# Kernel tuning notes

Hardware: AMD Instinct MI355X
Metric: run time of the kernel (lower is better)

## Reference

```python
import jax, jax.numpy as jnp
import numpy as np

DIM = 1024
HEADS = 16
HEAD_DIM = DIM // HEADS
B, S = 4, 2048


def setup_inputs() -> dict:
    key = jax.random.key(0)
    ks = jax.random.split(key, 12)
    scale = 1.0 / np.sqrt(DIM)
    inp = {
        "q": jax.random.normal(ks[0], (B, S, DIM), jnp.float32),
        "k": jax.random.normal(ks[1], (B, S, DIM), jnp.float32),
        "v": jax.random.normal(ks[2], (B, S, DIM), jnp.float32),
        "Wq": jax.random.normal(ks[3], (DIM, DIM), jnp.float32) * scale,
        "bq": jax.random.normal(ks[4], (DIM,), jnp.float32) * 0.01,
        "Wk": jax.random.normal(ks[5], (DIM, DIM), jnp.float32) * scale,
        "bk": jax.random.normal(ks[6], (DIM,), jnp.float32) * 0.01,
        "Wv": jax.random.normal(ks[7], (DIM, DIM), jnp.float32) * scale,
        "bv": jax.random.normal(ks[8], (DIM,), jnp.float32) * 0.01,
        "Wo": jax.random.normal(ks[9], (DIM, DIM), jnp.float32) * scale,
        "bo": jax.random.normal(ks[10], (DIM,), jnp.float32) * 0.01,
        "mask": jax.random.randint(ks[11], (B, S, S), 0, 2, jnp.int32),
    }
    return inp


def reference(q, k, v, Wq, bq, Wk, bk, Wv, bv, Wo, bo, mask):
    # QKV projections, split into heads: [B, H, S, Dh]
    def proj(x, W, b):
        y = x @ W + b
        return y.reshape(B, S, HEADS, HEAD_DIM).transpose(0, 2, 1, 3)

    qh, kh, vh = proj(q, Wq, bq), proj(k, Wk, bk), proj(v, Wv, bv)

    # scaled dot-product attention with additive mask fill (-1e9 where mask==0)
    score = jnp.einsum('bhqd,bhkd->bhqk', qh, kh) / jnp.sqrt(jnp.float32(HEAD_DIM))
    score = jnp.where(mask[:, None, :, :] == 0, jnp.float32(-1e9), score)
    attn = jax.nn.softmax(score, axis=-1)  # dropout p=0.0 -> identity

    out = jnp.einsum('bhqk,bhkd->bhqd', attn, vh)
    out = out.transpose(0, 2, 1, 3).reshape(B, S, DIM)
    return out @ Wo + bo
```

## Files before the change

### kernel.cpp

```cpp
#include <hip/hip_runtime.h>
#include <cstdint>
#include <cstddef>

#define BB 4
#define SS 2048
#define DIMM 1024
#define NH 16
#define DH 64
#define MT 8192

typedef __attribute__((ext_vector_type(8))) short bf16x8;
typedef __attribute__((ext_vector_type(4))) float f32x4;
typedef __attribute__((ext_vector_type(4))) unsigned short u16x4;
typedef __attribute__((ext_vector_type(4))) unsigned int uint32x4;

#define MFMA_BF16(a, b, c) __builtin_amdgcn_mfma_f32_16x16x32_bf16(a, b, c, 0, 0, 0)

#define QSCALE 0.1803368801111137f

__device__ __forceinline__ unsigned int cvtpk(float lo, float hi) {
    unsigned int r;
    asm("v_cvt_pk_bf16_f32 %0, %1, %2" : "=v"(r) : "v"(lo), "v"(hi));
    return r;
}

__device__ __forceinline__ unsigned short f2b1(float f) {
    return (unsigned short)cvtpk(f, f);
}

__device__ __forceinline__ float fexp2(float x) {
    float r;
    asm("v_exp_f32 %0, %1" : "=v"(r) : "v"(x));
    return r;
}

__device__ __forceinline__ void gload16(const void* g, void* l) {
    __builtin_amdgcn_global_load_lds(
        (const __attribute__((address_space(1))) unsigned int*)g,
        (__attribute__((address_space(3))) unsigned int*)l, 16, 0, 0);
}

__device__ __forceinline__ int swzb(int row, int cb) {
    return row * 128 + (((cb) ^ (row & 7)) << 4);
}

__global__ __launch_bounds__(256)
void prep_kernel(const float* __restrict__ q, const float* __restrict__ k,
                 const float* __restrict__ v,
                 unsigned short* __restrict__ Qb, unsigned short* __restrict__ Kb,
                 unsigned short* __restrict__ Vb,
                 const int* __restrict__ mask, unsigned long long* __restrict__ mp,
                 const float* __restrict__ Wq, const float* __restrict__ Wk,
                 const float* __restrict__ Wv, const float* __restrict__ Wo,
                 unsigned short* __restrict__ WT3, unsigned short* __restrict__ WTo)
{
    __shared__ unsigned short T[64][72];
    const int tid = threadIdx.x;
    const int bid = blockIdx.x;

    if (bid < 12288) {
        const int which = bid >> 12;
        const float* src = (which == 0) ? q : (which == 1) ? k : v;
        unsigned short* dst = (which == 0) ? Qb : (which == 1) ? Kb : Vb;
        const size_t i = ((size_t)(bid & 4095) * 256 + tid) * 8;
        const float4 lo = *reinterpret_cast<const float4*>(src + i);
        const float4 hi = *reinterpret_cast<const float4*>(src + i + 4);
        uint32x4 w = {cvtpk(lo.x, lo.y), cvtpk(lo.z, lo.w),
                      cvtpk(hi.x, hi.y), cvtpk(hi.z, hi.w)};
        *reinterpret_cast<uint32x4*>(dst + i) = w;
    } else if (bid < 77824) {
        const size_t i = (size_t)(bid - 12288) * 256 + tid;
        const unsigned long long bal = __ballot(mask[i] != 0);
        if ((tid & 63) == 0) mp[i >> 6] = bal;
    } else {
        const int wb = bid - 77824;
        const int which = wb >> 8;
        const float* W = (which == 0) ? Wq : (which == 1) ? Wk : (which == 2) ? Wv : Wo;
        unsigned short* WT = (which < 3) ? (WT3 + (size_t)which * DIMM * DIMM) : WTo;
        const float scale = (which == 0) ? QSCALE : 1.0f;
        const int within = wb & 255;
        const int n0 = (within & 15) * 64, k0 = (within >> 4) * 64;
#pragma unroll
        for (int it = 0; it < 4; ++it) {
            const int c = tid + it * 256;
            const int row = c >> 4, c4 = (c & 15) * 4;
            const float4 vv = *reinterpret_cast<const float4*>(
                &W[(size_t)(k0 + row) * DIMM + n0 + c4]);
            T[row][c4 + 0] = f2b1(vv.x * scale);
            T[row][c4 + 1] = f2b1(vv.y * scale);
            T[row][c4 + 2] = f2b1(vv.z * scale);
            T[row][c4 + 3] = f2b1(vv.w * scale);
        }
        __syncthreads();
#pragma unroll
        for (int it = 0; it < 4; ++it) {
            const int c = tid + it * 256;
            const int n = c >> 4, k4 = (c & 15) * 4;
            u16x4 o;
            o[0] = T[k4 + 0][n];
            o[1] = T[k4 + 1][n];
            o[2] = T[k4 + 2][n];
            o[3] = T[k4 + 3][n];
            *reinterpret_cast<u16x4*>(&WT[(size_t)(n0 + n) * DIMM + k0 + k4]) = o;
        }
    }
}

__global__ __launch_bounds__(256)
void gemm_qkv_kernel(const unsigned short* __restrict__ Qb,
                     const unsigned short* __restrict__ Kb,
                     const unsigned short* __restrict__ Vb,
                     const unsigned short* __restrict__ WT3,
                     const float* __restrict__ bq, const float* __restrict__ bk,
                     const float* __restrict__ bv,
                     unsigned short* __restrict__ Qh, unsigned short* __restrict__ Kh,
                     unsigned short* __restrict__ VhT)
{
    __shared__ __align__(16) unsigned short As[128 * 32];
    __shared__ __align__(16) unsigned short Bs[128 * 32];
    const int tid = threadIdx.x;
    const int w = tid >> 6, l = tid & 63;
    const int g = l >> 4, li = l & 15;
    const int bid = blockIdx.x;
    const int region = bid >> 9;
    const int rl = bid & 511;
    const int swz = (rl & 7) * 64 + (rl >> 3);
    const int m0 = (swz >> 3) * 128, n0 = (swz & 7) * 128;
    const int wm0 = (w >> 1) * 64, wn0 = (w & 1) * 64;

    const unsigned short* A = (region == 0) ? Qb : (region == 1) ? Kb : Vb;
    const unsigned short* BT = WT3 + (size_t)region * (DIMM * DIMM);

    const f32x4 fzero = {0.f, 0.f, 0.f, 0.f};
    f32x4 acc[4][4];
#pragma unroll
    for (int i = 0; i < 4; ++i)
#pragma unroll
        for (int j = 0; j < 4; ++j) acc[i][j] = fzero;

    for (int k0 = 0; k0 < DIMM; k0 += 32) {
#pragma unroll
        for (int it = 0; it < 2; ++it) {
            const int c = it * 256 + w * 64 + l;
            const int row = c >> 2, cb = c & 3;
            gload16(&A[(size_t)(m0 + row) * DIMM + k0 + cb * 8],
                    &As[(it * 256 + w * 64) * 8]);
        }
#pragma unroll
        for (int it = 0; it < 2; ++it) {
            const int c = it * 256 + w * 64 + l;
            const int row = c >> 2, cb = c & 3;
            gload16(&BT[(size_t)(n0 + row) * DIMM + k0 + cb * 8],
                    &Bs[(it * 256 + w * 64) * 8]);
        }
        __syncthreads();

        bf16x8 af[4], bf[4];
#pragma unroll
        for (int mb = 0; mb < 4; ++mb)
            af[mb] = *reinterpret_cast<const bf16x8*>(&As[(wm0 + mb * 16 + li) * 32 + g * 8]);
#pragma unroll
        for (int nb = 0; nb < 4; ++nb)
            bf[nb] = *reinterpret_cast<const bf16x8*>(&Bs[(wn0 + nb * 16 + li) * 32 + g * 8]);
#pragma unroll
        for (int mb = 0; mb < 4; ++mb)
#pragma unroll
            for (int nb = 0; nb < 4; ++nb)
                acc[mb][nb] = MFMA_BF16(af[mb], bf[nb], acc[mb][nb]);
        __syncthreads();
    }

    const float* bias = (region == 0) ? bq : (region == 1) ? bk : bv;
    const float bscale = (region == 0) ? QSCALE : 1.0f;
    float bv4[4];
#pragma unroll
    for (int nb = 0; nb < 4; ++nb)
        bv4[nb] = bias[n0 + wn0 + nb * 16 + li] * bscale;

    unsigned short* dst = (region == 0) ? Qh : (region == 1) ? Kh : VhT;
#pragma unroll
    for (int mb = 0; mb < 4; ++mb) {
#pragma unroll
        for (int r = 0; r < 4; ++r) {
            const int row_g = m0 + wm0 + mb * 16 + g * 4 + r;
#pragma unroll
            for (int nb = 0; nb < 4; ++nb) {
                const int col = n0 + wn0 + nb * 16 + li;
                const float val = acc[mb][nb][r] + bv4[nb];
                const int bb = row_g >> 11, s = row_g & 2047;
                const int hh = col >> 6, dd = col & 63;
                if (region < 2) {
                    dst[(((size_t)(bb * NH + hh)) * SS + s) * DH + dd] = f2b1(val);
                } else {
                    const int st = s & 63;
                    const int sp = (st & 32) + ((st >> 2) & 3) * 8 + ((st & 16) >> 2) + (st & 3);
                    dst[(((size_t)(bb * NH + hh)) * DH + dd) * SS + (s & ~63) + sp] = f2b1(val);
                }
            }
        }
    }
}

__global__ __launch_bounds__(256)
void gemm_out_kernel(const unsigned short* __restrict__ Ax, const unsigned short* __restrict__ BT,
                     const float* __restrict__ bias, float* __restrict__ Y)
{
    __shared__ __align__(16) unsigned short As[128 * 32];
    __shared__ __align__(16) unsigned short Bs[128 * 32];
    const int tid = threadIdx.x;
    const int w = tid >> 6, l = tid & 63;
    const int g = l >> 4, li = l & 15;
    const int bid = blockIdx.x;
    const int swz = (bid & 7) * 64 + (bid >> 3);
    const int m0 = (swz >> 3) * 128, n0 = (swz & 7) * 128;
    const int wm0 = (w >> 1) * 64, wn0 = (w & 1) * 64;

    const f32x4 fzero = {0.f, 0.f, 0.f, 0.f};
    f32x4 acc[4][4];
#pragma unroll
    for (int i = 0; i < 4; ++i)
#pragma unroll
        for (int j = 0; j < 4; ++j) acc[i][j] = fzero;

    for (int k0 = 0; k0 < DIMM; k0 += 32) {
        const int h = k0 >> 6;
#pragma unroll
        for (int it = 0; it < 2; ++it) {
            const int c = it * 256 + w * 64 + l;
            const int row = c >> 2, cb = c & 3;
            const int m = m0 + row;
            const int bb = m >> 11, s = m & 2047;
            gload16(&Ax[(((size_t)(bb * NH + h)) * SS + s) * DH + (k0 & 63) + cb * 8],
                    &As[(it * 256 + w * 64) * 8]);
        }
#pragma unroll
        for (int it = 0; it < 2; ++it) {
            const int c = it * 256 + w * 64 + l;
            const int row = c >> 2, cb = c & 3;
            gload16(&BT[(size_t)(n0 + row) * DIMM + k0 + cb * 8],
                    &Bs[(it * 256 + w * 64) * 8]);
        }
        __syncthreads();

        bf16x8 af[4], bf[4];
#pragma unroll
        for (int mb = 0; mb < 4; ++mb)
            af[mb] = *reinterpret_cast<const bf16x8*>(&As[(wm0 + mb * 16 + li) * 32 + g * 8]);
#pragma unroll
        for (int nb = 0; nb < 4; ++nb)
            bf[nb] = *reinterpret_cast<const bf16x8*>(&Bs[(wn0 + nb * 16 + li) * 32 + g * 8]);
#pragma unroll
        for (int mb = 0; mb < 4; ++mb)
#pragma unroll
            for (int nb = 0; nb < 4; ++nb)
                acc[mb][nb] = MFMA_BF16(af[mb], bf[nb], acc[mb][nb]);
        __syncthreads();
    }

    float bv4[4];
#pragma unroll
    for (int nb = 0; nb < 4; ++nb)
        bv4[nb] = bias[n0 + wn0 + nb * 16 + li];

#pragma unroll
    for (int mb = 0; mb < 4; ++mb) {
#pragma unroll
        for (int r = 0; r < 4; ++r) {
            const int row_g = m0 + wm0 + mb * 16 + g * 4 + r;
#pragma unroll
            for (int nb = 0; nb < 4; ++nb) {
                const int col = n0 + wn0 + nb * 16 + li;
                Y[(size_t)row_g * DIMM + col] = acc[mb][nb][r] + bv4[nb];
            }
        }
    }
}

__global__ __launch_bounds__(256, 4)
void flash_kernel(const unsigned short* __restrict__ Qh, const unsigned short* __restrict__ Kh,
                  const unsigned short* __restrict__ VhT, const unsigned long long* __restrict__ maskp,
                  unsigned short* __restrict__ Ctx)
{
    const int h = blockIdx.x, qt = blockIdx.y, b = blockIdx.z;
    const int tid = threadIdx.x;
    const int w = tid >> 6, l = tid & 63;
    const int g = l >> 4, li = l & 15;

    __shared__ __align__(16) unsigned short smem[4 * 64 * 64];
    __shared__ unsigned int LUT4[4];

    const int q0 = qt * 128;
    const size_t hb = ((size_t)(b * NH + h)) * (size_t)(SS * DH);

    if (tid < 4) LUT4[tid] = ((tid & 1) ? 0xFFFFu : 0u) | ((tid & 2) ? 0xFFFF0000u : 0u);

    bf16x8 qf[2][2];
#pragma unroll
    for (int qc = 0; qc < 2; ++qc) {
        const unsigned short* qp = &Qh[hb + (size_t)(q0 + w * 32 + qc * 16 + li) * DH + g * 8];
        qf[qc][0] = *reinterpret_cast<const bf16x8*>(qp);
        qf[qc][1] = *reinterpret_cast<const bf16x8*>(qp + 32);
    }

    bf16x8 vones;
#pragma unroll
    for (int j = 0; j < 8; ++j) vones[j] = (short)0x3F80;

    const f32x4 fzero = {0.f, 0.f, 0.f, 0.f};
    f32x4 oacc[2][4];
    f32x4 lacc[2];
#pragma unroll
    for (int qc = 0; qc < 2; ++qc) {
        lacc[qc] = fzero;
#pragma unroll
        for (int mb = 0; mb < 4; ++mb) oacc[qc][mb] = fzero;
    }

    int ks_[2], vs_[2];
#pragma unroll
    for (int it = 0; it < 2; ++it) {
        const int c = it * 256 + w * 64 + l;
        const int row = c >> 3, cb = (c & 7) ^ (row & 7);
        ks_[it] = row * DH + cb * 8;
        vs_[it] = row * SS + cb * 8;
    }
    const unsigned short* Ksrc = Kh + hb;
    const unsigned short* Vsrc = VhT + hb;
    const unsigned long long* mrow_p = maskp + ((size_t)(b * SS + q0 + w * 32 + li)) * 32;

#define STAGE(bn, tt) do {                                                      \
    gload16(Ksrc + (size_t)(tt) * 4096 + ks_[0], smem + (bn) * 4096 + w * 512); \
    gload16(Ksrc + (size_t)(tt) * 4096 + ks_[1], smem + (bn) * 4096 + 2048 + w * 512); \
    gload16(Vsrc + (size_t)(tt) * 64 + vs_[0], smem + 8192 + (bn) * 4096 + w * 512);   \
    gload16(Vsrc + (size_t)(tt) * 64 + vs_[1], smem + 8192 + (bn) * 4096 + 2048 + w * 512); \
} while (0)

    STAGE(0, 0);
    __syncthreads();

    int buf = 0;
    for (int t = 0; t < SS / 64; ++t) {
        if (t < SS / 64 - 1) STAGE(buf ^ 1, t + 1);

        const unsigned long long mw0 = mrow_p[t];
        const unsigned long long mw1 = mrow_p[512 + t];

        const char* Kc = (const char*)(smem + buf * 4096);
        bf16x8 kf[4][2];
#pragma unroll
        for (int nb = 0; nb < 4; ++nb)
#pragma unroll
            for (int hh = 0; hh < 2; ++hh)
                kf[nb][hh] = *reinterpret_cast<const bf16x8*>(
                    Kc + (nb * 16 + li) * 128 + (((hh * 4 + g) ^ (li & 7)) << 4));

        bf16x8 pf[2][2];
#pragma unroll
        for (int qc = 0; qc < 2; ++qc) {
            f32x4 st[4];
#pragma unroll
            for (int nb = 0; nb < 4; ++nb) st[nb] = fzero;
            __builtin_amdgcn_s_setprio(1);
#pragma unroll
            for (int nb = 0; nb < 4; ++nb)
#pragma unroll
                for (int hh = 0; hh < 2; ++hh)
                    st[nb] = MFMA_BF16(kf[nb][hh], qf[qc][hh], st[nb]);
            __builtin_amdgcn_s_setprio(0);

            float e[4][4];
#pragma unroll
            for (int nb = 0; nb < 4; ++nb)
#pragma unroll
                for (int r = 0; r < 4; ++r)
                    e[nb][r] = fexp2(st[nb][r]);

            const unsigned long long msh = (qc ? mw1 : mw0) >> (g * 4);
            const unsigned lo = (unsigned)msh, hi = (unsigned)(msh >> 32);
            uint32x4 w0 = {cvtpk(e[0][0], e[0][1]), cvtpk(e[0][2], e[0][3]),
                           cvtpk(e[1][0], e[1][1]), cvtpk(e[1][2], e[1][3])};
            uint32x4 w1 = {cvtpk(e[2][0], e[2][1]), cvtpk(e[2][2], e[2][3]),
                           cvtpk(e[3][0], e[3][1]), cvtpk(e[3][2], e[3][3])};
            w0[0] &= LUT4[lo & 3u];         w0[1] &= LUT4[(lo >> 2) & 3u];
            w0[2] &= LUT4[(lo >> 16) & 3u]; w0[3] &= LUT4[(lo >> 18) & 3u];
            w1[0] &= LUT4[hi & 3u];         w1[1] &= LUT4[(hi >> 2) & 3u];
            w1[2] &= LUT4[(hi >> 16) & 3u]; w1[3] &= LUT4[(hi >> 18) & 3u];
            pf[qc][0] = __builtin_bit_cast(bf16x8, w0);
            pf[qc][1] = __builtin_bit_cast(bf16x8, w1);
        }

        const char* Vc = (const char*)(smem + 8192 + buf * 4096);
        bf16x8 vf[4][2];
#pragma unroll
        for (int mb = 0; mb < 4; ++mb)
#pragma unroll
            for (int hh = 0; hh < 2; ++hh)
                vf[mb][hh] = *reinterpret_cast<const bf16x8*>(
                    Vc + (mb * 16 + li) * 128 + (((hh * 4 + g) ^ (li & 7)) << 4));

#pragma unroll
        for (int qc = 0; qc < 2; ++qc) {
            __builtin_amdgcn_s_setprio(1);
#pragma unroll
            for (int hh = 0; hh < 2; ++hh)
#pragma unroll
                for (int mb = 0; mb < 4; ++mb)
                    oacc[qc][mb] = MFMA_BF16(pf[qc][hh], vf[mb][hh], oacc[qc][mb]);
            lacc[qc] = MFMA_BF16(pf[qc][0], vones, lacc[qc]);
            lacc[qc] = MFMA_BF16(pf[qc][1], vones, lacc[qc]);
            __builtin_amdgcn_s_setprio(0);
        }

        __syncthreads();
        buf ^= 1;
    }
#undef STAGE

    unsigned short* Ps = smem;
#pragma unroll
    for (int qc = 0; qc < 2; ++qc) {
#pragma unroll
        for (int r = 0; r < 4; ++r) {
            const int row = w * 32 + qc * 16 + g * 4 + r;
            const float linv = 1.0f / lacc[qc][r];
#pragma unroll
            for (int mb = 0; mb < 4; ++mb) {
                const int dd = mb * 16 + li;
                *(unsigned short*)((char*)Ps + swzb(row, dd >> 3) + (dd & 7) * 2) =
                    f2b1(oacc[qc][mb][r] * linv);
            }
        }
    }
    __syncthreads();
#pragma unroll
    for (int it = 0; it < 4; ++it) {
        const int c = it * 64 + l;
        const int qrow = w * 32 + (c >> 3), cb = c & 7;
        const bf16x8 ov = *reinterpret_cast<const bf16x8*>((const char*)Ps + swzb(qrow, cb));
        *reinterpret_cast<bf16x8*>(&Ctx[hb + (size_t)(q0 + qrow) * DH + cb * 8]) = ov;
    }
}

extern "C" void kernel_launch(void* const* d_in, const int* in_sizes, int n_in,
                              void* d_out, int out_size, void* d_ws, size_t ws_size,
                              hipStream_t stream)
{
    const float* q  = (const float*)d_in[0];
    const float* k  = (const float*)d_in[1];
    const float* v  = (const float*)d_in[2];
    const float* Wq = (const float*)d_in[3];
    const float* bq = (const float*)d_in[4];
    const float* Wk = (const float*)d_in[5];
    const float* bk = (const float*)d_in[6];
    const float* Wv = (const float*)d_in[7];
    const float* bv = (const float*)d_in[8];
    const float* Wo = (const float*)d_in[9];
    const float* bo = (const float*)d_in[10];
    const int* mask = (const int*)d_in[11];
    float* out = (float*)d_out;

    const size_t M1 = 1048576, M8 = (size_t)MT * DIMM;
    unsigned short* WT3 = (unsigned short*)d_ws;
    unsigned short* WTo = WT3 + 3 * M1;
    unsigned short* Qb  = WTo + M1;
    unsigned short* Kb  = Qb + M8;
    unsigned short* Vb  = Kb + M8;
    unsigned short* Qh  = Vb + M8;
    unsigned short* Kh  = Qh + M8;
    unsigned long long* maskp = (unsigned long long*)(Kh + M8);
    unsigned short* VhT = (unsigned short*)(maskp + (size_t)BB * SS * SS / 64);
    unsigned short* Ctx = Kb;

    dim3 blk(256);

    prep_kernel<<<dim3(78848), blk, 0, stream>>>(q, k, v, Qb, Kb, Vb,
                                                 mask, maskp,
                                                 Wq, Wk, Wv, Wo, WT3, WTo);

    gemm_qkv_kernel<<<dim3(1536), blk, 0, stream>>>(Qb, Kb, Vb, WT3, bq, bk, bv,
                                                    Qh, Kh, VhT);

    dim3 fgrid(NH, SS / 128, BB);
    flash_kernel<<<fgrid, blk, 0, stream>>>(Qh, Kh, VhT, maskp, Ctx);

    gemm_out_kernel<<<dim3(512), blk, 0, stream>>>(Ctx, WTo, bo, out);
}
```

Measured before the change: 274.7 us.

## Drop LDS K/V staging in flash kernel, load fragments directly from global

New measurement: 639.2 us. 2.33x slower.

```diff
diff --git a/kernel.cpp b/kernel.cpp
--- a/kernel.cpp
+++ b/kernel.cpp
@@ -276,7 +276,7 @@
     }
 }
 
-__global__ __launch_bounds__(256, 4)
+__global__ __launch_bounds__(256, 5)
 void flash_kernel(const unsigned short* __restrict__ Qh, const unsigned short* __restrict__ Kh,
                   const unsigned short* __restrict__ VhT, const unsigned long long* __restrict__ maskp,
                   unsigned short* __restrict__ Ctx)
@@ -286,20 +286,20 @@
     const int w = tid >> 6, l = tid & 63;
     const int g = l >> 4, li = l & 15;
 
-    __shared__ __align__(16) unsigned short smem[4 * 64 * 64];
+    __shared__ __align__(16) unsigned short Ps[64 * 64];
     __shared__ unsigned int LUT4[4];
 
-    const int q0 = qt * 128;
+    const int q0 = qt * 64;
     const size_t hb = ((size_t)(b * NH + h)) * (size_t)(SS * DH);
 
     if (tid < 4) LUT4[tid] = ((tid & 1) ? 0xFFFFu : 0u) | ((tid & 2) ? 0xFFFF0000u : 0u);
-
-    bf16x8 qf[2][2];
-#pragma unroll
-    for (int qc = 0; qc < 2; ++qc) {
-        const unsigned short* qp = &Qh[hb + (size_t)(q0 + w * 32 + qc * 16 + li) * DH + g * 8];
-        qf[qc][0] = *reinterpret_cast<const bf16x8*>(qp);
-        qf[qc][1] = *reinterpret_cast<const bf16x8*>(qp + 32);
+    __syncthreads();
+
+    bf16x8 qf[2];
+    {
+        const unsigned short* qp = &Qh[hb + (size_t)(q0 + w * 16 + li) * DH + g * 8];
+        qf[0] = *reinterpret_cast<const bf16x8*>(qp);
+        qf[1] = *reinterpret_cast<const bf16x8*>(qp + 32);
     }
 
     bf16x8 vones;
@@ -307,135 +307,93 @@
     for (int j = 0; j < 8; ++j) vones[j] = (short)0x3F80;
 
     const f32x4 fzero = {0.f, 0.f, 0.f, 0.f};
-    f32x4 oacc[2][4];
-    f32x4 lacc[2];
-#pragma unroll
-    for (int qc = 0; qc < 2; ++qc) {
-        lacc[qc] = fzero;
-#pragma unroll
-        for (int mb = 0; mb < 4; ++mb) oacc[qc][mb] = fzero;
-    }
-
-    int ks_[2], vs_[2];
-#pragma unroll
-    for (int it = 0; it < 2; ++it) {
-        const int c = it * 256 + w * 64 + l;
-        const int row = c >> 3, cb = (c & 7) ^ (row & 7);
-        ks_[it] = row * DH + cb * 8;
-        vs_[it] = row * SS + cb * 8;
-    }
-    const unsigned short* Ksrc = Kh + hb;
-    const unsigned short* Vsrc = VhT + hb;
-    const unsigned long long* mrow_p = maskp + ((size_t)(b * SS + q0 + w * 32 + li)) * 32;
-
-#define STAGE(bn, tt) do {                                                      \
-    gload16(Ksrc + (size_t)(tt) * 4096 + ks_[0], smem + (bn) * 4096 + w * 512); \
-    gload16(Ksrc + (size_t)(tt) * 4096 + ks_[1], smem + (bn) * 4096 + 2048 + w * 512); \
-    gload16(Vsrc + (size_t)(tt) * 64 + vs_[0], smem + 8192 + (bn) * 4096 + w * 512);   \
-    gload16(Vsrc + (size_t)(tt) * 64 + vs_[1], smem + 8192 + (bn) * 4096 + 2048 + w * 512); \
-} while (0)
-
-    STAGE(0, 0);
-    __syncthreads();
-
-    int buf = 0;
+    f32x4 oacc[4];
+    f32x4 lacc = fzero;
+#pragma unroll
+    for (int mb = 0; mb < 4; ++mb) oacc[mb] = fzero;
+
+    const unsigned short* Kl = Kh + hb + (size_t)li * DH + g * 8;
+    const unsigned short* Vl = VhT + hb + (size_t)li * SS + g * 8;
+    const unsigned long long* mrow_p = maskp + ((size_t)(b * SS + q0 + w * 16 + li)) * 32;
+
     for (int t = 0; t < SS / 64; ++t) {
-        if (t < SS / 64 - 1) STAGE(buf ^ 1, t + 1);
-
-        const unsigned long long mw0 = mrow_p[t];
-        const unsigned long long mw1 = mrow_p[512 + t];
-
-        const char* Kc = (const char*)(smem + buf * 4096);
+        const unsigned long long mw = mrow_p[t];
+
+        const unsigned short* Kt = Kl + t * 4096;
         bf16x8 kf[4][2];
 #pragma unroll
         for (int nb = 0; nb < 4; ++nb)
 #pragma unroll
             for (int hh = 0; hh < 2; ++hh)
-                kf[nb][hh] = *reinterpret_cast<const bf16x8*>(
-                    Kc + (nb * 16 + li) * 128 + (((hh * 4 + g) ^ (li & 7)) << 4));
-
-        bf16x8 pf[2][2];
-#pragma unroll
-        for (int qc = 0; qc < 2; ++qc) {
-            f32x4 st[4];
-#pragma unroll
-            for (int nb = 0; nb < 4; ++nb) st[nb] = fzero;
-            __builtin_amdgcn_s_setprio(1);
-#pragma unroll
-            for (int nb = 0; nb < 4; ++nb)
-#pragma unroll
-                for (int hh = 0; hh < 2; ++hh)
-                    st[nb] = MFMA_BF16(kf[nb][hh], qf[qc][hh], st[nb]);
-            __builtin_amdgcn_s_setprio(0);
-
-            float e[4][4];
-#pragma unroll
-            for (int nb = 0; nb < 4; ++nb)
-#pragma unroll
-                for (int r = 0; r < 4; ++r)
-                    e[nb][r] = fexp2(st[nb][r]);
-
-            const unsigned long long msh = (qc ? mw1 : mw0) >> (g * 4);
-            const unsigned lo = (unsigned)msh, hi = (unsigned)(msh >> 32);
-            uint32x4 w0 = {cvtpk(e[0][0], e[0][1]), cvtpk(e[0][2], e[0][3]),
-                           cvtpk(e[1][0], e[1][1]), cvtpk(e[1][2], e[1][3])};
-            uint32x4 w1 = {cvtpk(e[2][0], e[2][1]), cvtpk(e[2][2], e[2][3]),
-                           cvtpk(e[3][0], e[3][1]), cvtpk(e[3][2], e[3][3])};
-            w0[0] &= LUT4[lo & 3u];         w0[1] &= LUT4[(lo >> 2) & 3u];
-            w0[2] &= LUT4[(lo >> 16) & 3u]; w0[3] &= LUT4[(lo >> 18) & 3u];
-            w1[0] &= LUT4[hi & 3u];         w1[1] &= LUT4[(hi >> 2) & 3u];
-            w1[2] &= LUT4[(hi >> 16) & 3u]; w1[3] &= LUT4[(hi >> 18) & 3u];
-            pf[qc][0] = __builtin_bit_cast(bf16x8, w0);
-            pf[qc][1] = __builtin_bit_cast(bf16x8, w1);
-        }
-
-        const char* Vc = (const char*)(smem + 8192 + buf * 4096);
+                kf[nb][hh] = *reinterpret_cast<const bf16x8*>(Kt + nb * 1024 + hh * 32);
+
+        f32x4 st[4];
+#pragma unroll
+        for (int nb = 0; nb < 4; ++nb) st[nb] = fzero;
+        __builtin_amdgcn_s_setprio(1);
+#pragma unroll
+        for (int nb = 0; nb < 4; ++nb)
+#pragma unroll
+            for (int hh = 0; hh < 2; ++hh)
+                st[nb] = MFMA_BF16(kf[nb][hh], qf[hh], st[nb]);
+        __builtin_amdgcn_s_setprio(0);
+
+        float e[4][4];
+#pragma unroll
+        for (int nb = 0; nb < 4; ++nb)
+#pragma unroll
+            for (int r = 0; r < 4; ++r)
+                e[nb][r] = fexp2(st[nb][r]);
+
+        const unsigned long long msh = mw >> (g * 4);
+        const unsigned lo = (unsigned)msh, hi = (unsigned)(msh >> 32);
+        uint32x4 w0 = {cvtpk(e[0][0], e[0][1]), cvtpk(e[0][2], e[0][3]),
+                       cvtpk(e[1][0], e[1][1]), cvtpk(e[1][2], e[1][3])};
+        uint32x4 w1 = {cvtpk(e[2][0], e[2][1]), cvtpk(e[2][2], e[2][3]),
+                       cvtpk(e[3][0], e[3][1]), cvtpk(e[3][2], e[3][3])};
+        w0[0] &= LUT4[lo & 3u];         w0[1] &= LUT4[(lo >> 2) & 3u];
+        w0[2] &= LUT4[(lo >> 16) & 3u]; w0[3] &= LUT4[(lo >> 18) & 3u];
+        w1[0] &= LUT4[hi & 3u];         w1[1] &= LUT4[(hi >> 2) & 3u];
+        w1[2] &= LUT4[(hi >> 16) & 3u]; w1[3] &= LUT4[(hi >> 18) & 3u];
+        bf16x8 pf[2];
+        pf[0] = __builtin_bit_cast(bf16x8, w0);
+        pf[1] = __builtin_bit_cast(bf16x8, w1);
+
+        const unsigned short* Vt = Vl + t * 64;
         bf16x8 vf[4][2];
 #pragma unroll
         for (int mb = 0; mb < 4; ++mb)
 #pragma unroll
             for (int hh = 0; hh < 2; ++hh)
                 vf[mb][hh] = *reinterpret_cast<const bf16x8*>(
-                    Vc + (mb * 16 + li) * 128 + (((hh * 4 + g) ^ (li & 7)) << 4));
-
-#pragma unroll
-        for (int qc = 0; qc < 2; ++qc) {
-            __builtin_amdgcn_s_setprio(1);
-#pragma unroll
-            for (int hh = 0; hh < 2; ++hh)
-#pragma unroll
-                for (int mb = 0; mb < 4; ++mb)
-                    oacc[qc][mb] = MFMA_BF16(pf[qc][hh], vf[mb][hh], oacc[qc][mb]);
-            lacc[qc] = MFMA_BF16(pf[qc][0], vones, lacc[qc]);
-            lacc[qc] = MFMA_BF16(pf[qc][1], vones, lacc[qc]);
-            __builtin_amdgcn_s_setprio(0);
-        }
-
-        __syncthreads();
-        buf ^= 1;
-    }
-#undef STAGE
-
-    unsigned short* Ps = smem;
-#pragma unroll
-    for (int qc = 0; qc < 2; ++qc) {
-#pragma unroll
-        for (int r = 0; r < 4; ++r) {
-            const int row = w * 32 + qc * 16 + g * 4 + r;
-            const float linv = 1.0f / lacc[qc][r];
-#pragma unroll
-            for (int mb = 0; mb < 4; ++mb) {
-                const int dd = mb * 16 + li;
-                *(unsigned short*)((char*)Ps + swzb(row, dd >> 3) + (dd & 7) * 2) =
-                    f2b1(oacc[qc][mb][r] * linv);
-            }
-        }
-    }
-    __syncthreads();
-#pragma unroll
-    for (int it = 0; it < 4; ++it) {
+                    Vt + (size_t)mb * 16 * SS + hh * 32);
+
+        __builtin_amdgcn_s_setprio(1);
+#pragma unroll
+        for (int hh = 0; hh < 2; ++hh)
+#pragma unroll
+            for (int mb = 0; mb < 4; ++mb)
+                oacc[mb] = MFMA_BF16(pf[hh], vf[mb][hh], oacc[mb]);
+        lacc = MFMA_BF16(pf[0], vones, lacc);
+        lacc = MFMA_BF16(pf[1], vones, lacc);
+        __builtin_amdgcn_s_setprio(0);
+    }
+
+#pragma unroll
+    for (int r = 0; r < 4; ++r) {
+        const int row = w * 16 + g * 4 + r;
+        const float linv = 1.0f / lacc[r];
+#pragma unroll
+        for (int mb = 0; mb < 4; ++mb) {
+            const int dd = mb * 16 + li;
+            *(unsigned short*)((char*)Ps + swzb(row, dd >> 3) + (dd & 7) * 2) =
+                f2b1(oacc[mb][r] * linv);
+        }
+    }
+#pragma unroll
+    for (int it = 0; it < 2; ++it) {
         const int c = it * 64 + l;
-        const int qrow = w * 32 + (c >> 3), cb = c & 7;
+        const int qrow = w * 16 + (c >> 3), cb = c & 7;
         const bf16x8 ov = *reinterpret_cast<const bf16x8*>((const char*)Ps + swzb(qrow, cb));
         *reinterpret_cast<bf16x8*>(&Ctx[hb + (size_t)(q0 + qrow) * DH + cb * 8]) = ov;
     }
@@ -480,7 +438,7 @@
     gemm_qkv_kernel<<<dim3(1536), blk, 0, stream>>>(Qb, Kb, Vb, WT3, bq, bk, bv,
                                                     Qh, Kh, VhT);
 
-    dim3 fgrid(NH, SS / 128, BB);
+    dim3 fgrid(NH, SS / 64, BB);
     flash_kernel<<<fgrid, blk, 0, stream>>>(Qh, Kh, VhT, maskp, Ctx);
 
     gemm_out_kernel<<<dim3(512), blk, 0, stream>>>(Ctx, WTo, bo, out);
```
